# Kernel tuning notes

Measured on AMD Instinct MI355X. Metric: run time of the kernel, lower is better.

The kernel has to match this reference:

```python
import jax, jax.numpy as jnp
import numpy as np

B, T = 2, 1024          # batch, seqlen (== block_size)
C = 512                 # n_embd
H, KV = 8, 2            # n_heads, n_kv_heads
HD = C // H             # head_dim = 64
L = 2                   # n_layers
E, K = 8, 2             # num_experts, num_experts_per_tok
V = 32000               # vocab_size
EPS = 1e-6


def setup_inputs() -> dict:
    key = jax.random.key(0)
    ks = jax.random.split(key, 12)
    s = 0.02
    return {
        "input_ids": jax.random.randint(ks[0], (B, T), 0, V, dtype=jnp.int32),
        "tok_emb": jax.random.normal(ks[1], (V, C), jnp.float32) * s,
        "pos_emb": jax.random.normal(ks[2], (T, C), jnp.float32) * s,
        "attn_norm_w": jnp.ones((L, C), jnp.float32),
        "q_w": jax.random.normal(ks[3], (L, C, C), jnp.float32) * s,
        "k_w": jax.random.normal(ks[4], (L, KV * HD, C), jnp.float32) * s,
        "v_w": jax.random.normal(ks[5], (L, KV * HD, C), jnp.float32) * s,
        "o_w": jax.random.normal(ks[6], (L, C, C), jnp.float32) * s,
        "ffn_norm_w": jnp.ones((L, C), jnp.float32),
        "gate_w": jax.random.normal(ks[7], (L, E, C), jnp.float32) * s,
        "expert_w": jax.random.normal(ks[8], (L, E, C, C), jnp.float32) * s,
        "final_norm_w": jnp.ones((C,), jnp.float32),
        "out_w": jax.random.normal(ks[9], (V, C), jnp.float32) * s,
    }


def rmsnorm(x, w):
    xf = x.astype(jnp.float32)
    n = xf * jax.lax.rsqrt(jnp.mean(xf * xf, axis=-1, keepdims=True) + EPS)
    return n.astype(x.dtype) * w


def gqa(x, qw, kw, vw, ow):
    b, t, _ = x.shape
    n_rep = H // KV
    xq = jnp.einsum('btc,dc->btd', x, qw).reshape(b, t, H, HD)
    xk = jnp.einsum('btc,dc->btd', x, kw).reshape(b, t, KV, HD)
    xv = jnp.einsum('btc,dc->btd', x, vw).reshape(b, t, KV, HD)
    xk = jnp.repeat(xk, n_rep, axis=2)  # repeat_interleave over head dim
    xv = jnp.repeat(xv, n_rep, axis=2)
    xq, xk, xv = (a.transpose(0, 2, 1, 3) for a in (xq, xk, xv))  # [b,h,t,hd]
    scores = jnp.einsum('bhqd,bhkd->bhqk', xq, xk) * (1.0 / HD ** 0.5)
    mask = jnp.tril(jnp.ones((t, t), bool))
    scores = jnp.where(mask, scores, jnp.float32(-1e30))
    attn = jax.nn.softmax(scores, axis=-1)
    out = jnp.einsum('bhqk,bhkd->bhqd', attn, xv)
    out = out.transpose(0, 2, 1, 3).reshape(b, t, C)
    return jnp.einsum('btc,dc->btd', out, ow)


def moe(x, gate_w, expert_w):
    b, t, c = x.shape
    xf = x.reshape(b * t, c)                                   # [N,C]
    logits = jnp.einsum('nc,ec->ne', xf, gate_w)               # [N,E]
    w, sel = jax.lax.top_k(logits, K)                          # [N,K]
    w = jax.nn.softmax(w.astype(jnp.float32), axis=-1).astype(x.dtype)
    # combine weight per (token, expert): sum over slots of one-hot * weight
    comb = jnp.sum(jax.nn.one_hot(sel, E, dtype=x.dtype) * w[..., None], axis=1)  # [N,E]
    all_out = jnp.einsum('nc,edc->ned', xf, expert_w)          # dense expert GEMMs
    out = jnp.einsum('ne,ned->nd', comb, all_out)
    return out.reshape(b, t, c)


def reference(input_ids, tok_emb, pos_emb, attn_norm_w, q_w, k_w, v_w, o_w,
              ffn_norm_w, gate_w, expert_w, final_norm_w, out_w):
    h = tok_emb[input_ids] + pos_emb[None, :input_ids.shape[1], :]
    for l in range(L):
        h = h + gqa(rmsnorm(h, attn_norm_w[l]), q_w[l], k_w[l], v_w[l], o_w[l])
        h = h + moe(rmsnorm(h, ffn_norm_w[l]), gate_w[l], expert_w[l])
    return jnp.einsum('btc,vc->btv', rmsnorm(h, final_norm_w), out_w)
```

## Files before the change

kernel.cpp:

```cpp
#include <hip/hip_runtime.h>
#include <hip/hip_bf16.h>


#define BT   2048
#define TSEQ 1024
#define CDIM 512
#define NKVD 128
#define NEXP 8
#define NVOC 32000

using bf16 = __hip_bfloat16;
typedef __attribute__((ext_vector_type(8))) short short8;
typedef __attribute__((ext_vector_type(4))) float floatx4;


__device__ inline void split8(const float* __restrict__ src, short8& hi, short8& lo) {
    float4 f0 = *reinterpret_cast<const float4*>(src);
    float4 f1 = *reinterpret_cast<const float4*>(src + 4);
    float v[8] = {f0.x, f0.y, f0.z, f0.w, f1.x, f1.y, f1.z, f1.w};
    #pragma unroll
    for (int j = 0; j < 8; ++j) {
        unsigned u = __builtin_bit_cast(unsigned, v[j]);
        hi[j] = (short)(u >> 16);
        float hf = __builtin_bit_cast(float, u & 0xffff0000u);
        float r = v[j] - hf;
        lo[j] = (short)(__builtin_bit_cast(unsigned, r) >> 16);
    }
}

__device__ inline short8 cvt8(const float* __restrict__ src) {
    float4 f0 = *reinterpret_cast<const float4*>(src);
    float4 f1 = *reinterpret_cast<const float4*>(src + 4);
    float v[8] = {f0.x, f0.y, f0.z, f0.w, f1.x, f1.y, f1.z, f1.w};
    short8 h;
    #pragma unroll
    for (int j = 0; j < 8; ++j) {
        unsigned u = __builtin_bit_cast(unsigned, v[j]);
        u = u + 0x7fffu + ((u >> 16) & 1u);
        h[j] = (short)(u >> 16);
    }
    return h;
}

__device__ inline unsigned short tobf(float f) {
    unsigned u = __builtin_bit_cast(unsigned, f);
    u = u + 0x7fffu + ((u >> 16) & 1u);
    return (unsigned short)(u >> 16);
}

__device__ inline void gload_lds16(const void* g, void* lds) {
    __builtin_amdgcn_global_load_lds(
        (const __attribute__((address_space(1))) unsigned int*)g,
        (__attribute__((address_space(3))) unsigned int*)lds, 16, 0, 0);
}

__global__ void embed_k(const int* __restrict__ ids, const float* __restrict__ tok,
                        const float* __restrict__ pos, float* __restrict__ h) {
    int n = blockIdx.x, t = threadIdx.x;
    int id = ids[n];
    int p = n & (TSEQ - 1);
    for (int c = t; c < CDIM; c += 256)
        h[(long)n * CDIM + c] = tok[(long)id * CDIM + c] + pos[(long)p * CDIM + c];
}

__global__ void rms_k(const float* __restrict__ x, const float* __restrict__ w,
                      float* __restrict__ out) {
    int n = blockIdx.x, t = threadIdx.x;
    const float* xr = x + (long)n * CDIM;
    float v0 = xr[t], v1 = xr[t + 256];
    float ss = v0 * v0 + v1 * v1;
    #pragma unroll
    for (int o = 32; o > 0; o >>= 1) ss += __shfl_down(ss, o);
    __shared__ float red[4];
    if ((t & 63) == 0) red[t >> 6] = ss;
    __syncthreads();
    float tot = red[0] + red[1] + red[2] + red[3];
    float rstd = 1.0f / sqrtf(tot * (1.0f / CDIM) + 1e-6f);
    out[(long)n * CDIM + t]       = v0 * rstd * w[t];
    out[(long)n * CDIM + t + 256] = v1 * rstd * w[t + 256];
}

__global__ void rmsbf_k(const float* __restrict__ x, const float* __restrict__ w,
                        unsigned short* __restrict__ out) {
    int n = blockIdx.x, t = threadIdx.x;
    const float* xr = x + (long)n * CDIM;
    float v0 = xr[t], v1 = xr[t + 256];
    float ss = v0 * v0 + v1 * v1;
    #pragma unroll
    for (int o = 32; o > 0; o >>= 1) ss += __shfl_down(ss, o);
    __shared__ float red[4];
    if ((t & 63) == 0) red[t >> 6] = ss;
    __syncthreads();
    float tot = red[0] + red[1] + red[2] + red[3];
    float rstd = 1.0f / sqrtf(tot * (1.0f / CDIM) + 1e-6f);
    out[(long)n * CDIM + t]       = tobf(v0 * rstd * w[t]);
    out[(long)n * CDIM + t + 256] = tobf(v1 * rstd * w[t + 256]);
}

__global__ void cvtw_k(const float* __restrict__ src, unsigned short* __restrict__ dst) {
    long i = ((long)blockIdx.x * 256 + threadIdx.x) * 8;
    short8 h = cvt8(src + i);
    *reinterpret_cast<short8*>(dst + i) = h;
}

template<int BM, int BN, bool SPLIT, bool ACCUM, bool SKIPUP, bool KCLIP>
__global__ __launch_bounds__(256, 2)
void gemm_f32(const float* __restrict__ A, const float* __restrict__ B,
              float* __restrict__ D, int M, int N, int Kd,
              int lda, int ldb, int ldd,
              long aBatch, long bBatch, int dDiv, long dOuter, long dInner)
{
    constexpr int BK = 64;
    constexpr int WM = BM / 2, WN = BN / 2;
    constexpr int TM = WM / 16, TN = WN / 16;
    constexpr int LDP = BK + 8;
    __shared__ bf16 AsH[BM][LDP];
    __shared__ bf16 BsH[BN][LDP];
    __shared__ bf16 AsL[SPLIT ? BM : 1][SPLIT ? LDP : 1];
    __shared__ bf16 BsL[SPLIT ? BN : 1][SPLIT ? LDP : 1];

    int z = blockIdx.z;
    const float* Ap = A + (long)z * aBatch;
    const float* Bp = B + (long)z * bBatch;
    long dOff = (long)(z / dDiv) * dOuter + (long)(z % dDiv) * dInner;
    int bm = blockIdx.y * BM;
    int bn = blockIdx.x * BN;
    if constexpr (SKIPUP) { if (bn > bm) return; }
    int tid = threadIdx.x;
    int wave = tid >> 6, lane = tid & 63;
    int wm = (wave >> 1) * WM, wn = (wave & 1) * WN;
    int lrow = lane & 15, quad = lane >> 4;

    floatx4 acc[TM][TN];
    #pragma unroll
    for (int i = 0; i < TM; ++i)
        #pragma unroll
        for (int j = 0; j < TN; ++j)
            acc[i][j] = (floatx4){0.f, 0.f, 0.f, 0.f};

    constexpr int ACH = BM * BK / (8 * 256);
    constexpr int BCH = BN * BK / (8 * 256);

    int kend = KCLIP ? min(Kd, bm + BM) : Kd;

    for (int k0 = 0; k0 < kend; k0 += BK) {
        #pragma unroll
        for (int i = 0; i < ACH; ++i) {
            int c = tid + i * 256;
            int r = c >> 3, c8 = (c & 7) << 3;
            const float* src = Ap + (long)(bm + r) * lda + k0 + c8;
            if constexpr (SPLIT) {
                short8 hi, lo;
                split8(src, hi, lo);
                *reinterpret_cast<short8*>(&AsH[r][c8]) = hi;
                *reinterpret_cast<short8*>(&AsL[r][c8]) = lo;
            } else {
                *reinterpret_cast<short8*>(&AsH[r][c8]) = cvt8(src);
            }
        }
        #pragma unroll
        for (int i = 0; i < BCH; ++i) {
            int c = tid + i * 256;
            int r = c >> 3, c8 = (c & 7) << 3;
            const float* src = Bp + (long)(bn + r) * ldb + k0 + c8;
            if constexpr (SPLIT) {
                short8 hi, lo;
                split8(src, hi, lo);
                *reinterpret_cast<short8*>(&BsH[r][c8]) = hi;
                *reinterpret_cast<short8*>(&BsL[r][c8]) = lo;
            } else {
                *reinterpret_cast<short8*>(&BsH[r][c8]) = cvt8(src);
            }
        }
        __syncthreads();
        #pragma unroll
        for (int kc = 0; kc < BK / 32; ++kc) {
            short8 ah[TM], bh[TN], al[TM], bl[TN];
            #pragma unroll
            for (int i = 0; i < TM; ++i) {
                ah[i] = *reinterpret_cast<const short8*>(&AsH[wm + i * 16 + lrow][kc * 32 + quad * 8]);
                if constexpr (SPLIT)
                    al[i] = *reinterpret_cast<const short8*>(&AsL[wm + i * 16 + lrow][kc * 32 + quad * 8]);
            }
            #pragma unroll
            for (int j = 0; j < TN; ++j) {
                bh[j] = *reinterpret_cast<const short8*>(&BsH[wn + j * 16 + lrow][kc * 32 + quad * 8]);
                if constexpr (SPLIT)
                    bl[j] = *reinterpret_cast<const short8*>(&BsL[wn + j * 16 + lrow][kc * 32 + quad * 8]);
            }
            #pragma unroll
            for (int i = 0; i < TM; ++i)
                #pragma unroll
                for (int j = 0; j < TN; ++j) {
                    acc[i][j] = __builtin_amdgcn_mfma_f32_16x16x32_bf16(ah[i], bh[j], acc[i][j], 0, 0, 0);
                    if constexpr (SPLIT) {
                        acc[i][j] = __builtin_amdgcn_mfma_f32_16x16x32_bf16(ah[i], bl[j], acc[i][j], 0, 0, 0);
                        acc[i][j] = __builtin_amdgcn_mfma_f32_16x16x32_bf16(al[i], bh[j], acc[i][j], 0, 0, 0);
                    }
                }
        }
        __syncthreads();
    }

    #pragma unroll
    for (int i = 0; i < TM; ++i)
        #pragma unroll
        for (int j = 0; j < TN; ++j) {
            int row = bm + wm + i * 16 + quad * 4;
            int col = bn + wn + j * 16 + lrow;
            #pragma unroll
            for (int r = 0; r < 4; ++r) {
                long idx = dOff + (long)(row + r) * ldd + col;
                if constexpr (ACCUM) D[idx] += acc[i][j][r];
                else                 D[idx]  = acc[i][j][r];
            }
        }
}

__global__ __launch_bounds__(256, 2)
void gemm_qkv(const float* __restrict__ A, const float* __restrict__ Bq,
              const float* __restrict__ Bk, const float* __restrict__ Bv,
              float* __restrict__ D)
{
    constexpr int BK = 64, LDP = 72;
    __shared__ bf16 AsH[64][LDP], AsL[64][LDP];
    __shared__ bf16 BsH[64][LDP], BsL[64][LDP];

    int bx = blockIdx.x;
    const float* Bp = (bx < 8)  ? Bq + (long)bx * 64 * CDIM
                    : (bx < 10) ? Bk + (long)(bx - 8) * 64 * CDIM
                                : Bv + (long)(bx - 10) * 64 * CDIM;
    int bm = blockIdx.y * 64;
    int bn = bx * 64;
    int tid = threadIdx.x;
    int wave = tid >> 6, lane = tid & 63;
    int wm = (wave >> 1) * 32, wn = (wave & 1) * 32;
    int lrow = lane & 15, quad = lane >> 4;

    floatx4 acc[2][2];
    #pragma unroll
    for (int i = 0; i < 2; ++i)
        #pragma unroll
        for (int j = 0; j < 2; ++j)
            acc[i][j] = (floatx4){0.f, 0.f, 0.f, 0.f};

    for (int k0 = 0; k0 < CDIM; k0 += BK) {
        #pragma unroll
        for (int i = 0; i < 2; ++i) {
            int c = tid + i * 256;
            int r = c >> 3, c8 = (c & 7) << 3;
            short8 hi, lo;
            split8(A + (long)(bm + r) * CDIM + k0 + c8, hi, lo);
            *reinterpret_cast<short8*>(&AsH[r][c8]) = hi;
            *reinterpret_cast<short8*>(&AsL[r][c8]) = lo;
            split8(Bp + (long)r * CDIM + k0 + c8, hi, lo);
            *reinterpret_cast<short8*>(&BsH[r][c8]) = hi;
            *reinterpret_cast<short8*>(&BsL[r][c8]) = lo;
        }
        __syncthreads();
        #pragma unroll
        for (int kc = 0; kc < 2; ++kc) {
            short8 ah[2], al[2], bh[2], bl[2];
            #pragma unroll
            for (int i = 0; i < 2; ++i) {
                ah[i] = *reinterpret_cast<const short8*>(&AsH[wm + i * 16 + lrow][kc * 32 + quad * 8]);
                al[i] = *reinterpret_cast<const short8*>(&AsL[wm + i * 16 + lrow][kc * 32 + quad * 8]);
                bh[i] = *reinterpret_cast<const short8*>(&BsH[wn + i * 16 + lrow][kc * 32 + quad * 8]);
                bl[i] = *reinterpret_cast<const short8*>(&BsL[wn + i * 16 + lrow][kc * 32 + quad * 8]);
            }
            #pragma unroll
            for (int i = 0; i < 2; ++i)
                #pragma unroll
                for (int j = 0; j < 2; ++j) {
                    acc[i][j] = __builtin_amdgcn_mfma_f32_16x16x32_bf16(ah[i], bh[j], acc[i][j], 0, 0, 0);
                    acc[i][j] = __builtin_amdgcn_mfma_f32_16x16x32_bf16(ah[i], bl[j], acc[i][j], 0, 0, 0);
                    acc[i][j] = __builtin_amdgcn_mfma_f32_16x16x32_bf16(al[i], bh[j], acc[i][j], 0, 0, 0);
                }
        }
        __syncthreads();
    }

    #pragma unroll
    for (int i = 0; i < 2; ++i)
        #pragma unroll
        for (int j = 0; j < 2; ++j) {
            int row = bm + wm + i * 16 + quad * 4;
            int col = bn + wn + j * 16 + lrow;
            #pragma unroll
            for (int r = 0; r < 4; ++r)
                D[(long)(row + r) * 768 + col] = acc[i][j][r];
        }
}

__global__ __launch_bounds__(256)
void gemm_vocab(const bf16* __restrict__ A, const bf16* __restrict__ B,
                float* __restrict__ D)
{
    constexpr int BK = 64;
    __shared__ __align__(16) bf16 As[2][128 * BK];
    __shared__ __align__(16) bf16 Bs[2][128 * BK];

    int id  = blockIdx.x;
    int swz = (id & 7) * 500 + (id >> 3);
    int bm  = (swz & 15) << 7;
    int bn  = (swz >> 4) << 7;

    int tid = threadIdx.x;
    int wave = tid >> 6, lane = tid & 63;
    int wm = (wave >> 1) << 6, wn = (wave & 1) << 6;
    int lrow = lane & 15, quad = lane >> 4;

    floatx4 acc[4][4];
    #pragma unroll
    for (int i = 0; i < 4; ++i)
        #pragma unroll
        for (int j = 0; j < 4; ++j)
            acc[i][j] = (floatx4){0.f, 0.f, 0.f, 0.f};

    const bf16* a0 = A + (long)bm * CDIM;
    const bf16* b0 = B + (long)bn * CDIM;

    auto stage = [&](int buf, int k0) {
        #pragma unroll
        for (int i = 0; i < 4; ++i) {
            int pb = wave * 4096 + i * 1024;
            int p  = pb + lane * 16;
            int r  = p >> 7;
            int c  = (p & 127) >> 1;
            gload_lds16(a0 + (long)r * CDIM + k0 + c, (char*)As[buf] + pb);
            gload_lds16(b0 + (long)r * CDIM + k0 + c, (char*)Bs[buf] + pb);
        }
    };

    stage(0, 0);
    __syncthreads();
    int cur = 0;
    constexpr int NT = CDIM / BK;
    for (int t = 0; t < NT; ++t) {
        if (t + 1 < NT) stage(cur ^ 1, (t + 1) * BK);
        #pragma unroll
        for (int kc = 0; kc < BK / 32; ++kc) {
            short8 ah[4], bh[4];
            #pragma unroll
            for (int i = 0; i < 4; ++i) {
                ah[i] = *reinterpret_cast<const short8*>(As[cur] + (wm + i * 16 + lrow) * BK + kc * 32 + quad * 8);
                bh[i] = *reinterpret_cast<const short8*>(Bs[cur] + (wn + i * 16 + lrow) * BK + kc * 32 + quad * 8);
            }
            #pragma unroll
            for (int i = 0; i < 4; ++i)
                #pragma unroll
                for (int j = 0; j < 4; ++j)
                    acc[i][j] = __builtin_amdgcn_mfma_f32_16x16x32_bf16(ah[i], bh[j], acc[i][j], 0, 0, 0);
        }
        __syncthreads();
        cur ^= 1;
    }

    #pragma unroll
    for (int i = 0; i < 4; ++i)
        #pragma unroll
        for (int j = 0; j < 4; ++j) {
            int row = bm + wm + i * 16 + quad * 4;
            int col = bn + wn + j * 16 + lrow;
            #pragma unroll
            for (int r = 0; r < 4; ++r)
                D[(long)(row + r) * NVOC + col] = acc[i][j][r];
        }
}


__global__ void packqk_k(const float* __restrict__ QKV, float* __restrict__ Qp,
                         float* __restrict__ Kp) {
    long id = (long)blockIdx.x * 256 + threadIdx.x;
    int d = id & 63;
    int t = (id >> 6) & (TSEQ - 1);
    int z = id >> 16;
    int b = z >> 3, hh = z & 7, kvh = hh >> 2;
    long src = (long)(b * TSEQ + t) * 768;
    Qp[id] = QKV[src + hh * 64 + d];
    Kp[id] = QKV[src + 512 + kvh * 64 + d];
}

__global__ void vtr_k(const float* __restrict__ QKV, float* __restrict__ Vt) {
    __shared__ float tile[64][65];
    int z = blockIdx.y, tt = blockIdx.x;
    int b = z >> 3, kvh = (z & 7) >> 2;
    int t0 = tt * 64;
    int tid = threadIdx.x;
    #pragma unroll
    for (int i = 0; i < 16; ++i) {
        int d = tid & 63, tl = i * 4 + (tid >> 6);
        tile[tl][d] = QKV[(long)(b * TSEQ + t0 + tl) * 768 + 640 + kvh * 64 + d];
    }
    __syncthreads();
    #pragma unroll
    for (int i = 0; i < 16; ++i) {
        int tl = tid & 63, d = i * 4 + (tid >> 6);
        Vt[((long)z * 64 + d) * TSEQ + t0 + tl] = tile[tl][d];
    }
}

__global__ void softmax_k(float* __restrict__ S) {
    int q = blockIdx.x, z = blockIdx.y, t = threadIdx.x;
    float* srow = S + ((long)z * TSEQ + q) * TSEQ;
    int len = q + 1;
    int wend = ((q >> 7) + 1) << 7;
    const float sc = 0.125f;
    float mx = -3.0e38f;
    for (int k = t; k < len; k += 256) mx = fmaxf(mx, srow[k]);
    #pragma unroll
    for (int o = 32; o > 0; o >>= 1) mx = fmaxf(mx, __shfl_down(mx, o));
    __shared__ float red[8];
    if ((t & 63) == 0) red[t >> 6] = mx;
    __syncthreads();
    mx = fmaxf(fmaxf(red[0], red[1]), fmaxf(red[2], red[3]));
    float sum = 0.f;
    for (int k = t; k < len; k += 256) sum += __expf((srow[k] - mx) * sc);
    #pragma unroll
    for (int o = 32; o > 0; o >>= 1) sum += __shfl_down(sum, o);
    if ((t & 63) == 0) red[4 + (t >> 6)] = sum;
    __syncthreads();
    float inv = 1.0f / (red[4] + red[5] + red[6] + red[7]);
    for (int k = t; k < wend; k += 256) {
        float p = (k < len) ? __expf((srow[k] - mx) * sc) * inv : 0.0f;
        srow[k] = p;
    }
}


__global__ void route_k(const float* __restrict__ h, const float* __restrict__ w,
                        const float* __restrict__ gw, float* __restrict__ comb,
                        float* __restrict__ xn) {
    int n = blockIdx.x, t = threadIdx.x;
    const float* xr = h + (long)n * CDIM;
    float v0 = xr[t], v1 = xr[t + 256];
    float ss = v0 * v0 + v1 * v1;
    #pragma unroll
    for (int o = 32; o > 0; o >>= 1) ss += __shfl_down(ss, o);
    __shared__ float rr[4];
    __shared__ float ac[4][8];
    if ((t & 63) == 0) rr[t >> 6] = ss;
    __syncthreads();
    float tot = rr[0] + rr[1] + rr[2] + rr[3];
    float rstd = 1.0f / sqrtf(tot * (1.0f / CDIM) + 1e-6f);
    float x0 = v0 * rstd * w[t], x1 = v1 * rstd * w[t + 256];
    xn[(long)n * CDIM + t]       = x0;
    xn[(long)n * CDIM + t + 256] = x1;
    float pe[NEXP];
    #pragma unroll
    for (int e = 0; e < NEXP; ++e)
        pe[e] = x0 * gw[e * CDIM + t] + x1 * gw[e * CDIM + t + 256];
    #pragma unroll
    for (int e = 0; e < NEXP; ++e)
        #pragma unroll
        for (int o = 32; o > 0; o >>= 1) pe[e] += __shfl_down(pe[e], o);
    if ((t & 63) == 0)
        #pragma unroll
        for (int e = 0; e < NEXP; ++e) ac[t >> 6][e] = pe[e];
    __syncthreads();
    if (t == 0) {
        float lg[NEXP];
        #pragma unroll
        for (int e = 0; e < NEXP; ++e) lg[e] = ac[0][e] + ac[1][e] + ac[2][e] + ac[3][e];
        int i1 = 0; float l1 = lg[0];
        #pragma unroll
        for (int e = 1; e < NEXP; ++e) if (lg[e] > l1) { l1 = lg[e]; i1 = e; }
        int i2 = -1; float l2 = -3.0e38f;
        #pragma unroll
        for (int e = 0; e < NEXP; ++e) if (e != i1 && lg[e] > l2) { l2 = lg[e]; i2 = e; }
        float e2 = __expf(l2 - l1);
        float dnm = 1.0f + e2;
        float* cr = comb + (long)n * NEXP;
        #pragma unroll
        for (int e = 0; e < NEXP; ++e) cr[e] = 0.f;
        cr[i1] = 1.0f / dnm;
        cr[i2] = e2 / dnm;
    }
}

__global__ void combine_k(float* __restrict__ h, const float* __restrict__ allout,
                          const float* __restrict__ comb) {
    int n = blockIdx.x, t = threadIdx.x;
    __shared__ float cw[NEXP];
    if (t < NEXP) cw[t] = comb[(long)n * NEXP + t];
    __syncthreads();
    for (int c = t; c < CDIM; c += 256) {
        float a = h[(long)n * CDIM + c];
        #pragma unroll
        for (int e = 0; e < NEXP; ++e) {
            float wv = cw[e];
            if (wv != 0.0f) a += wv * allout[((long)e * BT + n) * CDIM + c];
        }
        h[(long)n * CDIM + c] = a;
    }
}


extern "C" void kernel_launch(void* const* d_in, const int* in_sizes, int n_in,
                              void* d_out, int out_size, void* d_ws, size_t ws_size,
                              hipStream_t stream) {
    const int*   ids  = (const int*)d_in[0];
    const float* tok  = (const float*)d_in[1];
    const float* pos  = (const float*)d_in[2];
    const float* anw  = (const float*)d_in[3];
    const float* qw   = (const float*)d_in[4];
    const float* kw   = (const float*)d_in[5];
    const float* vw   = (const float*)d_in[6];
    const float* ow   = (const float*)d_in[7];
    const float* fnw  = (const float*)d_in[8];
    const float* gw   = (const float*)d_in[9];
    const float* ew   = (const float*)d_in[10];
    const float* finw = (const float*)d_in[11];
    const float* outw = (const float*)d_in[12];
    float* out = (float*)d_out;

    char* wsp = (char*)d_ws;
    auto alloc = [&](size_t bytes) -> char* {
        char* p = wsp;
        wsp += (bytes + 255) & ~(size_t)255;
        return p;
    };
    float* H    = (float*)alloc((size_t)BT * CDIM * 4);
    float* XN   = (float*)alloc((size_t)BT * CDIM * 4);
    float* QKV  = (float*)alloc((size_t)BT * 768 * 4);
    float* QP   = (float*)alloc((size_t)16 * TSEQ * 64 * 4);
    float* KP   = (float*)alloc((size_t)16 * TSEQ * 64 * 4);
    float* VT   = (float*)alloc((size_t)16 * TSEQ * 64 * 4);
    float* AOB  = (float*)alloc((size_t)BT * CDIM * 4);
    float* SS   = (float*)alloc((size_t)16 * TSEQ * TSEQ * 4);
    float* AOUT = (float*)alloc((size_t)NEXP * BT * CDIM * 4);
    float* COMB = (float*)alloc((size_t)BT * NEXP * 4);

    embed_k<<<dim3(BT), dim3(256), 0, stream>>>(ids, tok, pos, H);

    for (int l = 0; l < 2; ++l) {
        const float* qwl = qw + (long)l * CDIM * CDIM;
        const float* kwl = kw + (long)l * NKVD * CDIM;
        const float* vwl = vw + (long)l * NKVD * CDIM;
        const float* owl = ow + (long)l * CDIM * CDIM;
        const float* ewl = ew + (long)l * NEXP * CDIM * CDIM;

        rms_k<<<dim3(BT), dim3(256), 0, stream>>>(H, anw + l * CDIM, XN);
        gemm_qkv<<<dim3(12, 32), dim3(256), 0, stream>>>(XN, qwl, kwl, vwl, QKV);
        packqk_k<<<dim3(4096), dim3(256), 0, stream>>>(QKV, QP, KP);
        vtr_k<<<dim3(16, 16), dim3(256), 0, stream>>>(QKV, VT);
        gemm_f32<128,128,true,false,true,false><<<dim3(8,8,16), dim3(256), 0, stream>>>(
            QP, KP, SS, TSEQ, TSEQ, 64, 64, 64, TSEQ,
            (long)TSEQ * 64, (long)TSEQ * 64, 1, (long)TSEQ * TSEQ, 0);
        softmax_k<<<dim3(TSEQ, 16), dim3(256), 0, stream>>>(SS);
        gemm_f32<64,64,true,false,false,true><<<dim3(1,16,16), dim3(256), 0, stream>>>(
            SS, VT, AOB, TSEQ, 64, TSEQ, TSEQ, TSEQ, CDIM,
            (long)TSEQ * TSEQ, (long)64 * TSEQ, 8, (long)TSEQ * CDIM, 64);
        gemm_f32<64,64,true,true,false,false><<<dim3(8,32,1), dim3(256), 0, stream>>>(
            AOB, owl, H, BT, CDIM, CDIM, CDIM, CDIM, CDIM, 0, 0, 1, 0, 0);
        route_k<<<dim3(BT), dim3(256), 0, stream>>>(
            H, fnw + l * CDIM, gw + (long)l * NEXP * CDIM, COMB, XN);
        gemm_f32<128,128,true,false,false,false><<<dim3(4,16,8), dim3(256), 0, stream>>>(
            XN, ewl, AOUT, BT, CDIM, CDIM, CDIM, CDIM, CDIM,
            0, (long)CDIM * CDIM, 1, (long)BT * CDIM, 0);
        combine_k<<<dim3(BT), dim3(256), 0, stream>>>(H, AOUT, COMB);
    }

    unsigned short* OWB = (unsigned short*)SS;
    unsigned short* XNB = (unsigned short*)XN;
    rmsbf_k<<<dim3(BT), dim3(256), 0, stream>>>(H, finw, XNB);
    cvtw_k<<<dim3((NVOC * CDIM) / (256 * 8)), dim3(256), 0, stream>>>(outw, OWB);
    gemm_vocab<<<dim3(4000), dim3(256), 0, stream>>>((const bf16*)XNB, (const bf16*)OWB, out);
}
```

Measured before the change: 817.7 us.

## Route MoE tokens to per-expert lists and compute only selected experts

The router now appends each token to per-expert lists with atomic counters, and a new gathered GEMM computes expert outputs only for routed tokens instead of all eight experts densely. K and V are also packed once per KV head rather than replicated per query head, with the attention GEMMs indexing the shared KV buffer via a batch divisor. This cuts expert GEMM work to roughly a quarter and reduces KV pack traffic. The cost is atomics in routing, gathered row loads, and a simpler 64x64 tile without double buffering.

```diff
diff --git a/kernel.cpp b/kernel.cpp
--- a/kernel.cpp
+++ b/kernel.cpp
@@ -63,6 +63,10 @@
         h[(long)n * CDIM + c] = tok[(long)id * CDIM + c] + pos[(long)p * CDIM + c];
 }
 
+__global__ void zero_k(int* __restrict__ p) {
+    if (threadIdx.x < 16) p[threadIdx.x] = 0;
+}
+
 __global__ void rms_k(const float* __restrict__ x, const float* __restrict__ w,
                       float* __restrict__ out) {
     int n = blockIdx.x, t = threadIdx.x;
@@ -108,7 +112,7 @@
 void gemm_f32(const float* __restrict__ A, const float* __restrict__ B,
               float* __restrict__ D, int M, int N, int Kd,
               int lda, int ldb, int ldd,
-              long aBatch, long bBatch, int dDiv, long dOuter, long dInner)
+              long aBatch, long bBatch, int bDiv, int dDiv, long dOuter, long dInner)
 {
     constexpr int BK = 64;
     constexpr int WM = BM / 2, WN = BN / 2;
@@ -121,7 +125,7 @@
 
     int z = blockIdx.z;
     const float* Ap = A + (long)z * aBatch;
-    const float* Bp = B + (long)z * bBatch;
+    const float* Bp = B + (long)(z / bDiv) * bBatch;
     long dOff = (long)(z / dDiv) * dOuter + (long)(z % dDiv) * dInner;
     int bm = blockIdx.y * BM;
     int bn = blockIdx.x * BN;
@@ -292,6 +296,93 @@
         }
 }
 
+__global__ __launch_bounds__(256, 2)
+void gemm_moe(const float* __restrict__ A, const float* __restrict__ EW,
+              float* __restrict__ AOUT, const int* __restrict__ cnt,
+              const int* __restrict__ list)
+{
+    constexpr int BK = 64, LDP = 72;
+    __shared__ bf16 AsH[64][LDP], AsL[64][LDP];
+    __shared__ bf16 BsH[64][LDP], BsL[64][LDP];
+
+    int e = blockIdx.z;
+    int me = cnt[e];
+    int bm = blockIdx.y * 64;
+    if (bm >= me) return;
+    const int* lst = list + e * BT;
+    const float* Bp = EW + (long)e * CDIM * CDIM + (long)blockIdx.x * 64 * CDIM;
+
+    int tid = threadIdx.x;
+    int wave = tid >> 6, lane = tid & 63;
+    int wm = (wave >> 1) * 32, wn = (wave & 1) * 32;
+    int lrow = lane & 15, quad = lane >> 4;
+
+    int sr = tid >> 3;
+    int tok0 = lst[min(bm + sr,      me - 1)];
+    int tok1 = lst[min(bm + sr + 32, me - 1)];
+
+    floatx4 acc[2][2];
+    #pragma unroll
+    for (int i = 0; i < 2; ++i)
+        #pragma unroll
+        for (int j = 0; j < 2; ++j)
+            acc[i][j] = (floatx4){0.f, 0.f, 0.f, 0.f};
+
+    for (int k0 = 0; k0 < CDIM; k0 += BK) {
+        int c8 = (tid & 7) << 3;
+        short8 hi, lo;
+        split8(A + (long)tok0 * CDIM + k0 + c8, hi, lo);
+        *reinterpret_cast<short8*>(&AsH[sr][c8]) = hi;
+        *reinterpret_cast<short8*>(&AsL[sr][c8]) = lo;
+        split8(A + (long)tok1 * CDIM + k0 + c8, hi, lo);
+        *reinterpret_cast<short8*>(&AsH[sr + 32][c8]) = hi;
+        *reinterpret_cast<short8*>(&AsL[sr + 32][c8]) = lo;
+        split8(Bp + (long)sr * CDIM + k0 + c8, hi, lo);
+        *reinterpret_cast<short8*>(&BsH[sr][c8]) = hi;
+        *reinterpret_cast<short8*>(&BsL[sr][c8]) = lo;
+        split8(Bp + (long)(sr + 32) * CDIM + k0 + c8, hi, lo);
+        *reinterpret_cast<short8*>(&BsH[sr + 32][c8]) = hi;
+        *reinterpret_cast<short8*>(&BsL[sr + 32][c8]) = lo;
+        __syncthreads();
+        #pragma unroll
+        for (int kc = 0; kc < 2; ++kc) {
+            short8 ah[2], al[2], bh[2], bl[2];
+            #pragma unroll
+            for (int i = 0; i < 2; ++i) {
+                ah[i] = *reinterpret_cast<const short8*>(&AsH[wm + i * 16 + lrow][kc * 32 + quad * 8]);
+                al[i] = *reinterpret_cast<const short8*>(&AsL[wm + i * 16 + lrow][kc * 32 + quad * 8]);
+                bh[i] = *reinterpret_cast<const short8*>(&BsH[wn + i * 16 + lrow][kc * 32 + quad * 8]);
+                bl[i] = *reinterpret_cast<const short8*>(&BsL[wn + i * 16 + lrow][kc * 32 + quad * 8]);
+            }
+            #pragma unroll
+            for (int i = 0; i < 2; ++i)
+                #pragma unroll
+                for (int j = 0; j < 2; ++j) {
+                    acc[i][j] = __builtin_amdgcn_mfma_f32_16x16x32_bf16(ah[i], bh[j], acc[i][j], 0, 0, 0);
+                    acc[i][j] = __builtin_amdgcn_mfma_f32_16x16x32_bf16(ah[i], bl[j], acc[i][j], 0, 0, 0);
+                    acc[i][j] = __builtin_amdgcn_mfma_f32_16x16x32_bf16(al[i], bh[j], acc[i][j], 0, 0, 0);
+                }
+        }
+        __syncthreads();
+    }
+
+    #pragma unroll
+    for (int i = 0; i < 2; ++i) {
+        int rb = wm + i * 16 + quad * 4;
+        #pragma unroll
+        for (int r = 0; r < 4; ++r) {
+            int g = bm + rb + r;
+            if (g < me) {
+                int tok = lst[g];
+                float* drow = AOUT + ((long)e * BT + tok) * CDIM + blockIdx.x * 64;
+                #pragma unroll
+                for (int j = 0; j < 2; ++j)
+                    drow[wn + j * 16 + lrow] = acc[i][j][r];
+            }
+        }
+    }
+}
+
 __global__ __launch_bounds__(256)
 void gemm_vocab(const bf16* __restrict__ A, const bf16* __restrict__ B,
                 float* __restrict__ D)
@@ -369,34 +460,34 @@
 }
 
 
-__global__ void packqk_k(const float* __restrict__ QKV, float* __restrict__ Qp,
-                         float* __restrict__ Kp) {
+__global__ void packq_k(const float* __restrict__ QKV, float* __restrict__ Qp) {
     long id = (long)blockIdx.x * 256 + threadIdx.x;
     int d = id & 63;
     int t = (id >> 6) & (TSEQ - 1);
     int z = id >> 16;
-    int b = z >> 3, hh = z & 7, kvh = hh >> 2;
-    long src = (long)(b * TSEQ + t) * 768;
-    Qp[id] = QKV[src + hh * 64 + d];
-    Kp[id] = QKV[src + 512 + kvh * 64 + d];
-}
-
-__global__ void vtr_k(const float* __restrict__ QKV, float* __restrict__ Vt) {
+    int b = z >> 3, hh = z & 7;
+    Qp[id] = QKV[(long)(b * TSEQ + t) * 768 + hh * 64 + d];
+}
+
+__global__ void packkv_k(const float* __restrict__ QKV, float* __restrict__ Kp,
+                         float* __restrict__ Vt) {
     __shared__ float tile[64][65];
-    int z = blockIdx.y, tt = blockIdx.x;
-    int b = z >> 3, kvh = (z & 7) >> 2;
-    int t0 = tt * 64;
+    int zk = blockIdx.y;
+    int b = zk >> 1, kvh = zk & 1;
+    int t0 = blockIdx.x * 64;
     int tid = threadIdx.x;
     #pragma unroll
     for (int i = 0; i < 16; ++i) {
         int d = tid & 63, tl = i * 4 + (tid >> 6);
-        tile[tl][d] = QKV[(long)(b * TSEQ + t0 + tl) * 768 + 640 + kvh * 64 + d];
+        long src = (long)(b * TSEQ + t0 + tl) * 768;
+        tile[tl][d] = QKV[src + 640 + kvh * 64 + d];
+        Kp[((long)zk * TSEQ + t0 + tl) * 64 + d] = QKV[src + 512 + kvh * 64 + d];
     }
     __syncthreads();
     #pragma unroll
     for (int i = 0; i < 16; ++i) {
         int tl = tid & 63, d = i * 4 + (tid >> 6);
-        Vt[((long)z * 64 + d) * TSEQ + t0 + tl] = tile[tl][d];
+        Vt[((long)zk * 64 + d) * TSEQ + t0 + tl] = tile[tl][d];
     }
 }
 
@@ -430,7 +521,8 @@
 
 __global__ void route_k(const float* __restrict__ h, const float* __restrict__ w,
                         const float* __restrict__ gw, float* __restrict__ comb,
-                        float* __restrict__ xn) {
+                        float* __restrict__ xn, int* __restrict__ cnt,
+                        int* __restrict__ list) {
     int n = blockIdx.x, t = threadIdx.x;
     const float* xr = h + (long)n * CDIM;
     float v0 = xr[t], v1 = xr[t + 256];
@@ -475,6 +567,8 @@
         for (int e = 0; e < NEXP; ++e) cr[e] = 0.f;
         cr[i1] = 1.0f / dnm;
         cr[i2] = e2 / dnm;
+        int p = atomicAdd(&cnt[i1], 1); list[i1 * BT + p] = n;
+        p     = atomicAdd(&cnt[i2], 1); list[i2 * BT + p] = n;
     }
 }
 
@@ -524,14 +618,17 @@
     float* XN   = (float*)alloc((size_t)BT * CDIM * 4);
     float* QKV  = (float*)alloc((size_t)BT * 768 * 4);
     float* QP   = (float*)alloc((size_t)16 * TSEQ * 64 * 4);
-    float* KP   = (float*)alloc((size_t)16 * TSEQ * 64 * 4);
-    float* VT   = (float*)alloc((size_t)16 * TSEQ * 64 * 4);
+    float* KP   = (float*)alloc((size_t)4 * TSEQ * 64 * 4);
+    float* VT   = (float*)alloc((size_t)4 * TSEQ * 64 * 4);
     float* AOB  = (float*)alloc((size_t)BT * CDIM * 4);
     float* SS   = (float*)alloc((size_t)16 * TSEQ * TSEQ * 4);
     float* AOUT = (float*)alloc((size_t)NEXP * BT * CDIM * 4);
     float* COMB = (float*)alloc((size_t)BT * NEXP * 4);
+    int*   CNT  = (int*)alloc(16 * 4);
+    int*   LIST = (int*)alloc((size_t)NEXP * BT * 4);
 
     embed_k<<<dim3(BT), dim3(256), 0, stream>>>(ids, tok, pos, H);
+    zero_k<<<dim3(1), dim3(64), 0, stream>>>(CNT);
 
     for (int l = 0; l < 2; ++l) {
         const float* qwl = qw + (long)l * CDIM * CDIM;
@@ -542,22 +639,22 @@
 
         rms_k<<<dim3(BT), dim3(256), 0, stream>>>(H, anw + l * CDIM, XN);
         gemm_qkv<<<dim3(12, 32), dim3(256), 0, stream>>>(XN, qwl, kwl, vwl, QKV);
-        packqk_k<<<dim3(4096), dim3(256), 0, stream>>>(QKV, QP, KP);
-        vtr_k<<<dim3(16, 16), dim3(256), 0, stream>>>(QKV, VT);
+        packq_k<<<dim3(4096), dim3(256), 0, stream>>>(QKV, QP);
+        packkv_k<<<dim3(16, 4), dim3(256), 0, stream>>>(QKV, KP, VT);
         gemm_f32<128,128,true,false,true,false><<<dim3(8,8,16), dim3(256), 0, stream>>>(
             QP, KP, SS, TSEQ, TSEQ, 64, 64, 64, TSEQ,
-            (long)TSEQ * 64, (long)TSEQ * 64, 1, (long)TSEQ * TSEQ, 0);
+            (long)TSEQ * 64, (long)TSEQ * 64, 4, 1, (long)TSEQ * TSEQ, 0);
         softmax_k<<<dim3(TSEQ, 16), dim3(256), 0, stream>>>(SS);
         gemm_f32<64,64,true,false,false,true><<<dim3(1,16,16), dim3(256), 0, stream>>>(
             SS, VT, AOB, TSEQ, 64, TSEQ, TSEQ, TSEQ, CDIM,
-            (long)TSEQ * TSEQ, (long)64 * TSEQ, 8, (long)TSEQ * CDIM, 64);
+            (long)TSEQ * TSEQ, (long)64 * TSEQ, 4, 8, (long)TSEQ * CDIM, 64);
         gemm_f32<64,64,true,true,false,false><<<dim3(8,32,1), dim3(256), 0, stream>>>(
-            AOB, owl, H, BT, CDIM, CDIM, CDIM, CDIM, CDIM, 0, 0, 1, 0, 0);
+            AOB, owl, H, BT, CDIM, CDIM, CDIM, CDIM, CDIM, 0, 0, 1, 1, 0, 0);
         route_k<<<dim3(BT), dim3(256), 0, stream>>>(
-            H, fnw + l * CDIM, gw + (long)l * NEXP * CDIM, COMB, XN);
-        gemm_f32<128,128,true,false,false,false><<<dim3(4,16,8), dim3(256), 0, stream>>>(
-            XN, ewl, AOUT, BT, CDIM, CDIM, CDIM, CDIM, CDIM,
-            0, (long)CDIM * CDIM, 1, (long)BT * CDIM, 0);
+            H, fnw + l * CDIM, gw + (long)l * NEXP * CDIM, COMB, XN,
+            CNT + l * 8, LIST);
+        gemm_moe<<<dim3(8, 32, 8), dim3(256), 0, stream>>>(
+            XN, ewl, AOUT, CNT + l * 8, LIST);
         combine_k<<<dim3(BT), dim3(256), 0, stream>>>(H, AOUT, COMB);
     }
 
```

Measured after the change: 848.5 us. 1.04x slower.
